# Optimization experiments

Hardware: AMD Instinct MI355X
Metric: run time of the kernel (lower is better)

Reference implementation:

```python
import jax, jax.numpy as jnp
import numpy as np

N_NODES = 100000
N_EDGES = 1600000
IN_C, HID_C, OUT_C = 128, 128, 64


def setup_inputs() -> dict:
    key = jax.random.key(0)
    k = jax.random.split(key, 5)
    x = jax.random.normal(k[0], (N_NODES, IN_C), dtype=jnp.float32)
    edge_index = jax.random.randint(k[1], (2, N_EDGES), 0, N_NODES, dtype=jnp.int32)
    # Glorot-ish scaling for the GCNConv linear weights
    W1 = jax.random.normal(k[2], (IN_C, HID_C), dtype=jnp.float32) * (1.0 / np.sqrt(IN_C))
    b1 = jnp.zeros((HID_C,), dtype=jnp.float32)
    W2 = jax.random.normal(k[3], (HID_C, OUT_C), dtype=jnp.float32) * (1.0 / np.sqrt(HID_C))
    b2 = jnp.zeros((OUT_C,), dtype=jnp.float32)
    return {"x": x, "edge_index": edge_index, "W1": W1, "b1": b1, "W2": W2, "b2": b2}


def _gcn_conv(h, W, b, src, dst, deg_inv_sqrt, n):
    # h: [N, F_in] -> linear transform, then deg-normalized scatter-add over edges
    h = h @ W  # [N, F_out]
    norm = deg_inv_sqrt[src] * deg_inv_sqrt[dst]  # [E+N] (self-loops included)
    msgs = h[src] * norm[:, None]  # gather + scale
    out = jax.ops.segment_sum(msgs, dst, num_segments=n)  # scatter-add to dst
    return out + b


def reference(x, edge_index, W1, b1, W2, b2):
    n = x.shape[0]
    loops = jnp.arange(n, dtype=edge_index.dtype)
    src = jnp.concatenate([edge_index[0], loops])  # add self-loops (PyG default)
    dst = jnp.concatenate([edge_index[1], loops])
    deg = jax.ops.segment_sum(jnp.ones_like(dst, dtype=x.dtype), dst, num_segments=n)
    deg_inv_sqrt = jax.lax.rsqrt(deg)  # deg >= 1 due to self-loops

    h = _gcn_conv(x, W1, b1, src, dst, deg_inv_sqrt, n)
    h = jax.nn.relu(h)
    # F.dropout(training=False) is identity at inference
    h = _gcn_conv(h, W2, b2, src, dst, deg_inv_sqrt, n)
    return jax.nn.log_softmax(h, axis=1)
```

## Files before the change

kernel.cpp:

```cpp
#include <hip/hip_runtime.h>
#include <hip/hip_bf16.h>


typedef unsigned short ushortT;
typedef unsigned char ucharT;
typedef __attribute__((ext_vector_type(8))) short short8v;
typedef __attribute__((ext_vector_type(4))) float float4v;
typedef __attribute__((ext_vector_type(2))) float float2v;
typedef __attribute__((ext_vector_type(8))) unsigned short ushort8v;

__device__ __forceinline__ float bf2f(ushortT u) {
  union { unsigned int i; float f; } x;
  x.i = ((unsigned int)u) << 16;
  return x.f;
}

__device__ __forceinline__ ushortT f2bf(float f) {
  __hip_bfloat16 h = __float2bfloat16(f);
  return *(ushortT*)&h;
}

__device__ __forceinline__ ucharT f2fp8(float f) {
  unsigned int w = __builtin_amdgcn_cvt_pk_fp8_f32(f, f, 0, false);
  return (ucharT)(w & 0xff);
}

__device__ __forceinline__ bool probe_isbf(const void* xv) {
  const ushortT* xr = (const ushortT*)xv;
  const int lane = threadIdx.x & 63;
  float v = bf2f(xr[lane]);
  bool sane = isfinite(v) && fabsf(v) < 1e4f;
  return __ballot(sane) == ~0ull;
}

__global__ __launch_bounds__(256) void bhist_k(const int* __restrict__ dst, int E, int B,
                                               int* __restrict__ gbc,
                                               const void* __restrict__ W1v,
                                               const void* __restrict__ W2v,
                                               const void* __restrict__ xv,
                                               ushortT* __restrict__ Wt1,
                                               ushortT* __restrict__ Wt2,
                                               int* __restrict__ gcur) {
  __shared__ int h[512];
  const int tid = threadIdx.x;
  if (blockIdx.x == 0)
    for (int i = tid; i < 512; i += 256) gcur[i] = 0;
  const int gi = blockIdx.x * 256 + tid;
  if (gi < 24576) {
    const bool isbf = probe_isbf(xv);
    if (gi < 16384) {
      int nn = gi & 127, k = gi >> 7;
      ushortT v = isbf ? ((const ushortT*)W1v)[k * 128 + nn]
                       : f2bf(((const float*)W1v)[k * 128 + nn]);
      Wt1[nn * 128 + k] = v;
    } else {
      int j = gi - 16384;
      int nn = j & 63, k = j >> 6;
      ushortT v = isbf ? ((const ushortT*)W2v)[k * 64 + nn]
                       : f2bf(((const float*)W2v)[k * 64 + nn]);
      Wt2[nn * 128 + k] = v;
    }
  }
  for (int i = tid; i < B; i += 256) h[i] = 0;
  __syncthreads();
  const int i0 = blockIdx.x * 8192;
  const int iend = min(i0 + 8192, E);
  for (int i = i0 + tid; i < iend; i += 256) atomicAdd(&h[dst[i] >> 8], 1);
  __syncthreads();
  for (int i = tid; i < B; i += 256)
    if (h[i]) atomicAdd(&gbc[i], h[i]);
}

__global__ __launch_bounds__(256) void bin_k(const int* __restrict__ srcv,
                                             const int* __restrict__ dstv, int E, int B,
                                             const int* __restrict__ gbc,
                                             int* __restrict__ gcur,
                                             int* __restrict__ tmp) {
  __shared__ int hist[512];
  __shared__ int base[512];
  __shared__ int sbb[512];
  const int tid = threadIdx.x;
  {
    int a = (2 * tid < B) ? gbc[2 * tid] : 0;
    int b2 = (2 * tid + 1 < B) ? gbc[2 * tid + 1] : 0;
    const int sum = a + b2;
    hist[tid] = sum;
    __syncthreads();
    int run = sum;
    for (int off = 1; off < 256; off <<= 1) {
      int v = (tid >= off) ? hist[tid - off] : 0;
      __syncthreads();
      run += v;
      hist[tid] = run;
      __syncthreads();
    }
    const int excl = run - sum;
    if (2 * tid < B) sbb[2 * tid] = excl;
    if (2 * tid + 1 < B) sbb[2 * tid + 1] = excl + a;
    __syncthreads();
  }
  const int i0 = blockIdx.x * 8192;
  const int iend = min(i0 + 8192, E);
  for (int i = tid; i < B; i += 256) hist[i] = 0;
  __syncthreads();
  for (int i = i0 + tid; i < iend; i += 256) atomicAdd(&hist[dstv[i] >> 8], 1);
  __syncthreads();
  for (int i = tid; i < B; i += 256) {
    int h = hist[i];
    base[i] = h ? (sbb[i] + atomicAdd(&gcur[i], h)) : 0;
    hist[i] = 0;
  }
  __syncthreads();
  for (int i = i0 + tid; i < iend; i += 256) {
    int d = dstv[i];
    int s = srcv[i];
    int b = d >> 8;
    int l = atomicAdd(&hist[b], 1);
    tmp[base[b] + l] = s | ((d & 255) << 17);
  }
}

__global__ __launch_bounds__(256) void csr_k(const int* __restrict__ tmp,
                                             const int* __restrict__ gbc, int n,
                                             int2* __restrict__ rpc,
                                             float* __restrict__ dis,
                                             int* __restrict__ col) {
  __shared__ int lhist[256];
  __shared__ int lexcl[256];
  __shared__ int red[256];
  const int b = blockIdx.x;
  const int tid = threadIdx.x;
  int part = 0;
  for (int i = tid; i < b; i += 256) part += gbc[i];
  red[tid] = part;
  __syncthreads();
  for (int off = 128; off > 0; off >>= 1) {
    if (tid < off) red[tid] += red[tid + off];
    __syncthreads();
  }
  const int e0 = red[0];
  const int e1 = e0 + gbc[b];
  __syncthreads();
  lhist[tid] = 0;
  __syncthreads();
  for (int i = e0 + tid; i < e1; i += 256) atomicAdd(&lhist[tmp[i] >> 17], 1);
  __syncthreads();
  const int v = lhist[tid];
  int run = v;
  lexcl[tid] = run;
  __syncthreads();
  for (int off = 1; off < 256; off <<= 1) {
    int t = (tid >= off) ? lexcl[tid - off] : 0;
    __syncthreads();
    run += t;
    lexcl[tid] = run;
    __syncthreads();
  }
  const int excl = run - v;
  const int node = (b << 8) + tid;
  if (node < n) {
    rpc[node] = make_int2(e0 + excl, v);
    dis[node] = rsqrtf((float)(v + 1));
  }
  lhist[tid] = 0;
  lexcl[tid] = excl;
  __syncthreads();
  for (int i = e0 + tid; i < e1; i += 256) {
    int p = tmp[i];
    int dloc = p >> 17;
    int s = p & 131071;
    int l = atomicAdd(&lhist[dloc], 1);
    col[e0 + lexcl[dloc] + l] = s;
  }
}

__global__ __launch_bounds__(512) void gemm1_k(const void* __restrict__ xv,
                                               const ushortT* __restrict__ Wt1,
                                               const float* __restrict__ dis,
                                               ucharT* __restrict__ Hb8, int n) {
  __shared__ ushortT sW[128 * 132];
  const bool isbf = probe_isbf(xv);
  const int tid = threadIdx.x;
  for (int i = tid; i < 4096; i += 512) {
    int nn = i >> 5, k4 = (i & 31) * 4;
    *(ushort4*)&sW[nn * 132 + k4] = *(const ushort4*)&Wt1[nn * 128 + k4];
  }
  __syncthreads();

  const int wave = tid >> 6;
  const int lane = tid & 63;
  const int m = lane & 15;
  const int quad = lane >> 4;
  const int row = blockIdx.x * 128 + wave * 16 + m;
  const int rowc = min(row, n - 1);

  float4v acc[8];
#pragma unroll
  for (int t = 0; t < 8; ++t) acc[t] = (float4v)(0.f);

  if (isbf) {
    const ushortT* xp = (const ushortT*)xv + (size_t)rowc * 128 + quad * 8;
#pragma unroll
    for (int kc = 0; kc < 4; ++kc) {
      short8v af = *(const short8v*)(xp + kc * 32);
#pragma unroll
      for (int nb = 0; nb < 8; ++nb) {
        short8v bf = *(const short8v*)&sW[(nb * 16 + m) * 132 + kc * 32 + quad * 8];
        acc[nb] = __builtin_amdgcn_mfma_f32_16x16x32_bf16(af, bf, acc[nb], 0, 0, 0);
      }
    }
  } else {
    const float* xp = (const float*)xv + (size_t)rowc * 128 + quad * 8;
#pragma unroll
    for (int kc = 0; kc < 4; ++kc) {
      float4 lo = *(const float4*)(xp + kc * 32);
      float4 hi = *(const float4*)(xp + kc * 32 + 4);
      short8v af;
      af[0] = (short)f2bf(lo.x); af[1] = (short)f2bf(lo.y);
      af[2] = (short)f2bf(lo.z); af[3] = (short)f2bf(lo.w);
      af[4] = (short)f2bf(hi.x); af[5] = (short)f2bf(hi.y);
      af[6] = (short)f2bf(hi.z); af[7] = (short)f2bf(hi.w);
#pragma unroll
      for (int nb = 0; nb < 8; ++nb) {
        short8v bf = *(const short8v*)&sW[(nb * 16 + m) * 132 + kc * 32 + quad * 8];
        acc[nb] = __builtin_amdgcn_mfma_f32_16x16x32_bf16(af, bf, acc[nb], 0, 0, 0);
      }
    }
  }

#pragma unroll
  for (int r = 0; r < 4; ++r) {
    int grow = blockIdx.x * 128 + wave * 16 + quad * 4 + r;
    if (grow <= n) {
      float sc = (grow < n) ? dis[grow] : 0.f;
#pragma unroll
      for (int nb = 0; nb < 8; ++nb)
        Hb8[(size_t)grow * 128 + nb * 16 + m] =
            (grow < n) ? f2fp8(sc * acc[nb][r]) : (ucharT)0;
    }
  }
}

__global__ __launch_bounds__(256) void agg1_k(const ucharT* __restrict__ Hb8,
                                              const int* __restrict__ col,
                                              const int2* __restrict__ rpc,
                                              const float* __restrict__ dis,
                                              const void* __restrict__ b1v,
                                              const void* __restrict__ xv,
                                              ushortT* __restrict__ Ab, int n) {
  const bool isbf = probe_isbf(xv);
  const int tid = threadIdx.x;
  const int lane = tid & 63;
  const int wave = tid >> 6;
  const int quad = lane >> 4;
  const int o = (lane >> 3) & 1;
  const int c16 = (lane & 7) * 16;
  const int node = blockIdx.x * 16 + wave * 4 + quad;
  const bool valid = node < n;
  const int nd = valid ? node : (n - 1);

  const int2 rc = rpc[nd];
  const int start = rc.x;
  const int cnt = valid ? rc.y : 0;
  const float din = dis[nd];

  const uint4 hsp = *(const uint4*)&Hb8[((unsigned)(valid ? node : n) << 7) + (unsigned)c16];
  float b[16];
  if (isbf) {
    ushort8v b0 = *(const ushort8v*)((const ushortT*)b1v + c16);
    ushort8v b1 = *(const ushort8v*)((const ushortT*)b1v + c16 + 8);
#pragma unroll
    for (int k = 0; k < 8; ++k) { b[k] = bf2f(b0[k]); b[8 + k] = bf2f(b1[k]); }
  } else {
    const float* bf = (const float*)b1v + c16;
#pragma unroll
    for (int k = 0; k < 16; ++k) b[k] = bf[k];
  }

  int cmax = cnt;
  cmax = max(cmax, __shfl_xor(cmax, 16));
  cmax = max(cmax, __shfl_xor(cmax, 32));
  const int cmaxs = __builtin_amdgcn_readfirstlane(cmax);

  float2v acc[8];
#pragma unroll
  for (int k = 0; k < 8; ++k) acc[k] = (float2v)(0.f);

  int nxt[4];
#pragma unroll
  for (int u = 0; u < 4; ++u) nxt[u] = col[start + 2 * u + o];
  for (int e = 0; e < cmaxs; e += 8) {
    int cur[4];
#pragma unroll
    for (int u = 0; u < 4; ++u) cur[u] = nxt[u];
#pragma unroll
    for (int u = 0; u < 4; ++u) nxt[u] = col[start + e + 8 + 2 * u + o];
#pragma unroll
    for (int u = 0; u < 4; ++u) {
      const int ee = e + 2 * u + o;
      int s = (ee < cnt) ? cur[u] : n;
      const uint4 h = *(const uint4*)&Hb8[((unsigned)s << 7) + (unsigned)c16];
      acc[0] += __builtin_amdgcn_cvt_pk_f32_fp8(h.x, false);
      acc[1] += __builtin_amdgcn_cvt_pk_f32_fp8(h.x, true);
      acc[2] += __builtin_amdgcn_cvt_pk_f32_fp8(h.y, false);
      acc[3] += __builtin_amdgcn_cvt_pk_f32_fp8(h.y, true);
      acc[4] += __builtin_amdgcn_cvt_pk_f32_fp8(h.z, false);
      acc[5] += __builtin_amdgcn_cvt_pk_f32_fp8(h.z, true);
      acc[6] += __builtin_amdgcn_cvt_pk_f32_fp8(h.w, false);
      acc[7] += __builtin_amdgcn_cvt_pk_f32_fp8(h.w, true);
    }
  }

#pragma unroll
  for (int k = 0; k < 8; ++k) {
    float t0 = __shfl_xor(acc[k][0], 8);
    float t1 = __shfl_xor(acc[k][1], 8);
    acc[k][0] += t0;
    acc[k][1] += t1;
  }

  if (valid && o == 0) {
    float hs[16];
    {
      const unsigned int w4[4] = {hsp.x, hsp.y, hsp.z, hsp.w};
#pragma unroll
      for (int w = 0; w < 4; ++w) {
        float2v p0 = __builtin_amdgcn_cvt_pk_f32_fp8(w4[w], false);
        float2v p1 = __builtin_amdgcn_cvt_pk_f32_fp8(w4[w], true);
        hs[4 * w] = p0[0]; hs[4 * w + 1] = p0[1];
        hs[4 * w + 2] = p1[0]; hs[4 * w + 3] = p1[1];
      }
    }
    ushort8v o0, o1;
#pragma unroll
    for (int k = 0; k < 4; ++k) {
      o0[2 * k]     = f2bf(fmaxf(fmaf(din, acc[k][0] + hs[2 * k],     b[2 * k]),     0.f));
      o0[2 * k + 1] = f2bf(fmaxf(fmaf(din, acc[k][1] + hs[2 * k + 1], b[2 * k + 1]), 0.f));
    }
#pragma unroll
    for (int k = 4; k < 8; ++k) {
      o1[2 * (k - 4)]     = f2bf(fmaxf(fmaf(din, acc[k][0] + hs[2 * k],     b[2 * k]),     0.f));
      o1[2 * (k - 4) + 1] = f2bf(fmaxf(fmaf(din, acc[k][1] + hs[2 * k + 1], b[2 * k + 1]), 0.f));
    }
    *(ushort8v*)&Ab[(size_t)node * 128 + c16] = o0;
    *(ushort8v*)&Ab[(size_t)node * 128 + c16 + 8] = o1;
  }
}

__global__ __launch_bounds__(512) void gemm2_k(const ushortT* __restrict__ Ab,
                                               const ushortT* __restrict__ Wt2,
                                               const float* __restrict__ dis,
                                               ucharT* __restrict__ H2b8, int n) {
  __shared__ ushortT sW[64 * 132];
  const int tid = threadIdx.x;
  for (int i = tid; i < 2048; i += 512) {
    int nn = i >> 5, k4 = (i & 31) * 4;
    *(ushort4*)&sW[nn * 132 + k4] = *(const ushort4*)&Wt2[nn * 128 + k4];
  }
  __syncthreads();

  const int wave = tid >> 6;
  const int lane = tid & 63;
  const int m = lane & 15;
  const int quad = lane >> 4;
  const int row = blockIdx.x * 128 + wave * 16 + m;
  const int rowc = min(row, n - 1);

  float4v acc[4];
#pragma unroll
  for (int t = 0; t < 4; ++t) acc[t] = (float4v)(0.f);

  const ushortT* ap = Ab + (size_t)rowc * 128 + quad * 8;
#pragma unroll
  for (int kc = 0; kc < 4; ++kc) {
    short8v af = *(const short8v*)(ap + kc * 32);
#pragma unroll
    for (int nb = 0; nb < 4; ++nb) {
      short8v bf = *(const short8v*)&sW[(nb * 16 + m) * 132 + kc * 32 + quad * 8];
      acc[nb] = __builtin_amdgcn_mfma_f32_16x16x32_bf16(af, bf, acc[nb], 0, 0, 0);
    }
  }

#pragma unroll
  for (int r = 0; r < 4; ++r) {
    int grow = blockIdx.x * 128 + wave * 16 + quad * 4 + r;
    if (grow <= n) {
      float sc = (grow < n) ? dis[grow] : 0.f;
#pragma unroll
      for (int nb = 0; nb < 4; ++nb)
        H2b8[(size_t)grow * 64 + nb * 16 + m] =
            (grow < n) ? f2fp8(sc * acc[nb][r]) : (ucharT)0;
    }
  }
}

__global__ __launch_bounds__(256) void agg2_k(const ucharT* __restrict__ H2b8,
                                              const int* __restrict__ col,
                                              const int2* __restrict__ rpc,
                                              const float* __restrict__ dis,
                                              const void* __restrict__ b2v,
                                              const void* __restrict__ xv,
                                              void* __restrict__ outv, int n) {
  const bool isbf = probe_isbf(xv);
  const int tid = threadIdx.x;
  const int lane = tid & 63;
  const int wave = tid >> 6;
  const int quad = lane >> 4;
  const int o = (lane >> 3) & 1;
  const int c8 = (lane & 7) * 8;
  const int node = blockIdx.x * 16 + wave * 4 + quad;
  const bool valid = node < n;
  const int nd = valid ? node : (n - 1);

  const int2 rc = rpc[nd];
  const int start = rc.x;
  const int cnt = valid ? rc.y : 0;
  const float din = dis[nd];

  const uint2 hsp =
      *(const uint2*)&H2b8[((unsigned)(valid ? node : n) << 6) + (unsigned)c8];
  float b[8];
  if (isbf) {
    ushort8v bb = *(const ushort8v*)((const ushortT*)b2v + c8);
#pragma unroll
    for (int k = 0; k < 8; ++k) b[k] = bf2f(bb[k]);
  } else {
    const float* bf = (const float*)b2v + c8;
#pragma unroll
    for (int k = 0; k < 8; ++k) b[k] = bf[k];
  }

  int cmax = cnt;
  cmax = max(cmax, __shfl_xor(cmax, 16));
  cmax = max(cmax, __shfl_xor(cmax, 32));
  const int cmaxs = __builtin_amdgcn_readfirstlane(cmax);

  float2v acc[4];
#pragma unroll
  for (int k = 0; k < 4; ++k) acc[k] = (float2v)(0.f);

  int nxt[4];
#pragma unroll
  for (int u = 0; u < 4; ++u) nxt[u] = col[start + 2 * u + o];
  for (int e = 0; e < cmaxs; e += 8) {
    int cur[4];
#pragma unroll
    for (int u = 0; u < 4; ++u) cur[u] = nxt[u];
#pragma unroll
    for (int u = 0; u < 4; ++u) nxt[u] = col[start + e + 8 + 2 * u + o];
#pragma unroll
    for (int u = 0; u < 4; ++u) {
      const int ee = e + 2 * u + o;
      int s = (ee < cnt) ? cur[u] : n;
      const uint2 h = *(const uint2*)&H2b8[((unsigned)s << 6) + (unsigned)c8];
      acc[0] += __builtin_amdgcn_cvt_pk_f32_fp8(h.x, false);
      acc[1] += __builtin_amdgcn_cvt_pk_f32_fp8(h.x, true);
      acc[2] += __builtin_amdgcn_cvt_pk_f32_fp8(h.y, false);
      acc[3] += __builtin_amdgcn_cvt_pk_f32_fp8(h.y, true);
    }
  }

#pragma unroll
  for (int k = 0; k < 4; ++k) {
    float t0 = __shfl_xor(acc[k][0], 8);
    float t1 = __shfl_xor(acc[k][1], 8);
    acc[k][0] += t0;
    acc[k][1] += t1;
  }

  float hs[8];
  {
    float2v p0 = __builtin_amdgcn_cvt_pk_f32_fp8(hsp.x, false);
    float2v p1 = __builtin_amdgcn_cvt_pk_f32_fp8(hsp.x, true);
    float2v p2 = __builtin_amdgcn_cvt_pk_f32_fp8(hsp.y, false);
    float2v p3 = __builtin_amdgcn_cvt_pk_f32_fp8(hsp.y, true);
    hs[0] = p0[0]; hs[1] = p0[1]; hs[2] = p1[0]; hs[3] = p1[1];
    hs[4] = p2[0]; hs[5] = p2[1]; hs[6] = p3[0]; hs[7] = p3[1];
  }
  float v[8];
#pragma unroll
  for (int k = 0; k < 4; ++k) {
    v[2 * k]     = fmaf(din, acc[k][0] + hs[2 * k],     b[2 * k]);
    v[2 * k + 1] = fmaf(din, acc[k][1] + hs[2 * k + 1], b[2 * k + 1]);
  }

  float mx = v[0];
#pragma unroll
  for (int k = 1; k < 8; ++k) mx = fmaxf(mx, v[k]);
  for (int off = 1; off < 8; off <<= 1) mx = fmaxf(mx, __shfl_xor(mx, off));
  float ssum = 0.f;
#pragma unroll
  for (int k = 0; k < 8; ++k) ssum += __expf(v[k] - mx);
  for (int off = 1; off < 8; off <<= 1) ssum += __shfl_xor(ssum, off);
  const float lse = mx + __logf(ssum);

  if (valid && o == 0) {
    if (isbf) {
      ushort8v ov;
#pragma unroll
      for (int k = 0; k < 8; ++k) ov[k] = f2bf(v[k] - lse);
      *(ushort8v*)((__hip_bfloat16*)outv + (size_t)node * 64 + c8) = ov;
    } else {
      float4 o0 = make_float4(v[0] - lse, v[1] - lse, v[2] - lse, v[3] - lse);
      float4 o1 = make_float4(v[4] - lse, v[5] - lse, v[6] - lse, v[7] - lse);
      *(float4*)((float*)outv + (size_t)node * 64 + c8) = o0;
      *(float4*)((float*)outv + (size_t)node * 64 + c8 + 4) = o1;
    }
  }
}


extern "C" void kernel_launch(void* const* d_in, const int* in_sizes, int n_in,
                              void* d_out, int out_size, void* d_ws, size_t ws_size,
                              hipStream_t stream) {
  const void* x  = d_in[0];
  const int*  ei = (const int*)d_in[1];
  const void* W1 = d_in[2];
  const void* b1 = d_in[3];
  const void* W2 = d_in[4];
  const void* b2 = d_in[5];

  const int n = in_sizes[0] / 128;
  const int E = in_sizes[1] / 2;
  const int B = (n + 255) >> 8;
  const int* srcv = ei;
  const int* dstv = ei + E;

  char* p = (char*)d_ws;
  auto alloc = [&](size_t bytes) {
    char* q = p;
    p += (bytes + 255) & ~(size_t)255;
    return q;
  };
  ucharT* Hb8 = (ucharT*)alloc((size_t)(n + 1) * 128);
  ucharT* H2b8 = (ucharT*)alloc((size_t)(n + 1) * 64);
  ushortT* Ab = (ushortT*)alloc((size_t)n * 128 * 2);
  float* dis = (float*)alloc((size_t)n * 4);
  int2* rpc = (int2*)alloc((size_t)n * 8);
  int* gbc = (int*)alloc(512 * 4);
  int* gcur = (int*)alloc(512 * 4);
  ushortT* Wt1 = (ushortT*)alloc(16384 * 2);
  ushortT* Wt2 = (ushortT*)alloc(8192 * 2);
  int* tmp = (int*)alloc((size_t)E * 4);
  int* col = (int*)alloc(((size_t)E + 4096) * 4);

  (void)hipMemsetAsync(gbc, 0, 512 * sizeof(int), stream);

  const int gChunks = (E + 8191) / 8192;

  bhist_k<<<gChunks, 256, 0, stream>>>(dstv, E, B, gbc, W1, W2, x, Wt1, Wt2, gcur);
  bin_k<<<gChunks, 256, 0, stream>>>(srcv, dstv, E, B, gbc, gcur, tmp);
  csr_k<<<B, 256, 0, stream>>>(tmp, gbc, n, rpc, dis, col);

  gemm1_k<<<(n + 128) / 128, 512, 0, stream>>>(x, Wt1, dis, Hb8, n);
  agg1_k<<<(n + 15) / 16, 256, 0, stream>>>(Hb8, col, rpc, dis, b1, x, Ab, n);
  gemm2_k<<<(n + 128) / 128, 512, 0, stream>>>(Ab, Wt2, dis, H2b8, n);
  agg2_k<<<(n + 15) / 16, 256, 0, stream>>>(H2b8, col, rpc, dis, b2, x, d_out, n);
}
```

Baseline: 229.7 us.

## Replace bucketed two-pass CSR build with per-node atomic count and scatter

```diff
diff --git a/kernel.cpp b/kernel.cpp
--- a/kernel.cpp
+++ b/kernel.cpp
@@ -33,19 +33,14 @@
   return __ballot(sane) == ~0ull;
 }
 
-__global__ __launch_bounds__(256) void bhist_k(const int* __restrict__ dst, int E, int B,
-                                               int* __restrict__ gbc,
+__global__ __launch_bounds__(256) void bhist_k(const int* __restrict__ dst, int E,
                                                const void* __restrict__ W1v,
                                                const void* __restrict__ W2v,
                                                const void* __restrict__ xv,
                                                ushortT* __restrict__ Wt1,
                                                ushortT* __restrict__ Wt2,
-                                               int* __restrict__ gcur) {
-  __shared__ int h[512];
-  const int tid = threadIdx.x;
-  if (blockIdx.x == 0)
-    for (int i = tid; i < 512; i += 256) gcur[i] = 0;
-  const int gi = blockIdx.x * 256 + tid;
+                                               int* __restrict__ ncnt) {
+  const int gi = blockIdx.x * 256 + threadIdx.x;
   if (gi < 24576) {
     const bool isbf = probe_isbf(xv);
     if (gi < 16384) {
@@ -61,77 +56,20 @@
       Wt2[nn * 128 + k] = v;
     }
   }
-  for (int i = tid; i < B; i += 256) h[i] = 0;
-  __syncthreads();
-  const int i0 = blockIdx.x * 8192;
-  const int iend = min(i0 + 8192, E);
-  for (int i = i0 + tid; i < iend; i += 256) atomicAdd(&h[dst[i] >> 8], 1);
-  __syncthreads();
-  for (int i = tid; i < B; i += 256)
-    if (h[i]) atomicAdd(&gbc[i], h[i]);
-}
-
-__global__ __launch_bounds__(256) void bin_k(const int* __restrict__ srcv,
-                                             const int* __restrict__ dstv, int E, int B,
-                                             const int* __restrict__ gbc,
-                                             int* __restrict__ gcur,
-                                             int* __restrict__ tmp) {
-  __shared__ int hist[512];
-  __shared__ int base[512];
-  __shared__ int sbb[512];
-  const int tid = threadIdx.x;
-  {
-    int a = (2 * tid < B) ? gbc[2 * tid] : 0;
-    int b2 = (2 * tid + 1 < B) ? gbc[2 * tid + 1] : 0;
-    const int sum = a + b2;
-    hist[tid] = sum;
-    __syncthreads();
-    int run = sum;
-    for (int off = 1; off < 256; off <<= 1) {
-      int v = (tid >= off) ? hist[tid - off] : 0;
-      __syncthreads();
-      run += v;
-      hist[tid] = run;
-      __syncthreads();
-    }
-    const int excl = run - sum;
-    if (2 * tid < B) sbb[2 * tid] = excl;
-    if (2 * tid + 1 < B) sbb[2 * tid + 1] = excl + a;
-    __syncthreads();
-  }
-  const int i0 = blockIdx.x * 8192;
-  const int iend = min(i0 + 8192, E);
-  for (int i = tid; i < B; i += 256) hist[i] = 0;
-  __syncthreads();
-  for (int i = i0 + tid; i < iend; i += 256) atomicAdd(&hist[dstv[i] >> 8], 1);
-  __syncthreads();
-  for (int i = tid; i < B; i += 256) {
-    int h = hist[i];
-    base[i] = h ? (sbb[i] + atomicAdd(&gcur[i], h)) : 0;
-    hist[i] = 0;
-  }
-  __syncthreads();
-  for (int i = i0 + tid; i < iend; i += 256) {
-    int d = dstv[i];
-    int s = srcv[i];
-    int b = d >> 8;
-    int l = atomicAdd(&hist[b], 1);
-    tmp[base[b] + l] = s | ((d & 255) << 17);
-  }
-}
-
-__global__ __launch_bounds__(256) void csr_k(const int* __restrict__ tmp,
-                                             const int* __restrict__ gbc, int n,
-                                             int2* __restrict__ rpc,
-                                             float* __restrict__ dis,
-                                             int* __restrict__ col) {
-  __shared__ int lhist[256];
-  __shared__ int lexcl[256];
+  if (gi < E) atomicAdd(&ncnt[dst[gi]], 1);
+}
+
+__global__ __launch_bounds__(256) void rp_k(const int* __restrict__ ncnt, int n,
+                                            int2* __restrict__ rpc,
+                                            float* __restrict__ dis,
+                                            int* __restrict__ curp) {
   __shared__ int red[256];
+  __shared__ int sc[256];
   const int b = blockIdx.x;
   const int tid = threadIdx.x;
+  const int node = (b << 8) + tid;
   int part = 0;
-  for (int i = tid; i < b; i += 256) part += gbc[i];
+  for (int i = tid; i < (b << 8); i += 256) part += ncnt[i];
   red[tid] = part;
   __syncthreads();
   for (int off = 128; off > 0; off >>= 1) {
@@ -139,39 +77,36 @@
     __syncthreads();
   }
   const int e0 = red[0];
-  const int e1 = e0 + gbc[b];
-  __syncthreads();
-  lhist[tid] = 0;
-  __syncthreads();
-  for (int i = e0 + tid; i < e1; i += 256) atomicAdd(&lhist[tmp[i] >> 17], 1);
-  __syncthreads();
-  const int v = lhist[tid];
+  const int v = (node < n) ? ncnt[node] : 0;
   int run = v;
-  lexcl[tid] = run;
+  sc[tid] = run;
   __syncthreads();
   for (int off = 1; off < 256; off <<= 1) {
-    int t = (tid >= off) ? lexcl[tid - off] : 0;
+    int t = (tid >= off) ? sc[tid - off] : 0;
     __syncthreads();
     run += t;
-    lexcl[tid] = run;
+    sc[tid] = run;
     __syncthreads();
   }
   const int excl = run - v;
-  const int node = (b << 8) + tid;
   if (node < n) {
-    rpc[node] = make_int2(e0 + excl, v);
+    const int rowp = e0 + excl;
+    rpc[node] = make_int2(rowp, v);
     dis[node] = rsqrtf((float)(v + 1));
-  }
-  lhist[tid] = 0;
-  lexcl[tid] = excl;
-  __syncthreads();
-  for (int i = e0 + tid; i < e1; i += 256) {
-    int p = tmp[i];
-    int dloc = p >> 17;
-    int s = p & 131071;
-    int l = atomicAdd(&lhist[dloc], 1);
-    col[e0 + lexcl[dloc] + l] = s;
-  }
+    curp[node] = rowp;
+  }
+}
+
+__global__ __launch_bounds__(256) void scat_k(const int* __restrict__ srcv,
+                                              const int* __restrict__ dstv, int E,
+                                              int* __restrict__ curp,
+                                              int* __restrict__ col) {
+  const int i = blockIdx.x * 256 + threadIdx.x;
+  if (i >= E) return;
+  const int d = dstv[i];
+  const int s = srcv[i];
+  const int slot = atomicAdd(&curp[d], 1);
+  col[slot] = s;
 }
 
 __global__ __launch_bounds__(512) void gemm1_k(const void* __restrict__ xv,
@@ -537,20 +472,20 @@
   ushortT* Ab = (ushortT*)alloc((size_t)n * 128 * 2);
   float* dis = (float*)alloc((size_t)n * 4);
   int2* rpc = (int2*)alloc((size_t)n * 8);
-  int* gbc = (int*)alloc(512 * 4);
-  int* gcur = (int*)alloc(512 * 4);
+  int* ncnt = (int*)alloc((size_t)B * 256 * 4);
+  int* curp = (int*)alloc((size_t)n * 4);
   ushortT* Wt1 = (ushortT*)alloc(16384 * 2);
   ushortT* Wt2 = (ushortT*)alloc(8192 * 2);
-  int* tmp = (int*)alloc((size_t)E * 4);
   int* col = (int*)alloc(((size_t)E + 4096) * 4);
 
-  (void)hipMemsetAsync(gbc, 0, 512 * sizeof(int), stream);
-
-  const int gChunks = (E + 8191) / 8192;
-
-  bhist_k<<<gChunks, 256, 0, stream>>>(dstv, E, B, gbc, W1, W2, x, Wt1, Wt2, gcur);
-  bin_k<<<gChunks, 256, 0, stream>>>(srcv, dstv, E, B, gbc, gcur, tmp);
-  csr_k<<<B, 256, 0, stream>>>(tmp, gbc, n, rpc, dis, col);
+  (void)hipMemsetAsync(ncnt, 0, (size_t)B * 256 * sizeof(int), stream);
+
+  const int eBlocks = (E + 255) / 256;
+  const int hBlocks = max(eBlocks, 96);
+
+  bhist_k<<<hBlocks, 256, 0, stream>>>(dstv, E, W1, W2, x, Wt1, Wt2, ncnt);
+  rp_k<<<B, 256, 0, stream>>>(ncnt, n, rpc, dis, curp);
+  scat_k<<<eBlocks, 256, 0, stream>>>(srcv, dstv, E, curp, col);
 
   gemm1_k<<<(n + 128) / 128, 512, 0, stream>>>(x, Wt1, dis, Hb8, n);
   agg1_k<<<(n + 15) / 16, 256, 0, stream>>>(Hb8, col, rpc, dis, b1, x, Ab, n);
```

Measured after the change: 430.9 us. 87.6% more time.
